# Optimization experiments

Measured on AMD Instinct MI355X. Metric: run time of the kernel, lower is better.

## Reference

```python
import jax, jax.numpy as jnp
import numpy as np

MODE1 = 12
MODE2 = 12
WIDTH = 64
L = 10
DEPTH = 4
PAD = 9
EPS = 1e-5


def conv1x1(x, w, b):
    # x: (B,Ci,H,W), w: (Co,Ci), b: (Co,)
    return jnp.einsum('oi,bihw->bohw', w, x) + b[None, :, None, None]


def group_norm(x, gamma, beta, groups=2):
    B, C, H, W = x.shape
    xg = x.reshape(B, groups, C // groups, H, W)
    mu = xg.mean(axis=(2, 3, 4), keepdims=True)
    var = xg.var(axis=(2, 3, 4), keepdims=True)
    xn = ((xg - mu) * jax.lax.rsqrt(var + EPS)).reshape(B, C, H, W)
    return xn * gamma[None, :, None, None] + beta[None, :, None, None]


def spectral_conv(x, w1, w2):
    # x: (B,Ci,H,W); w1,w2: (Ci,Co,m1,m2,2) real/imag stacked
    B, Ci, H, W = x.shape
    Co = w1.shape[1]
    x_ft = jnp.fft.rfft2(x)  # (B,Ci,H,W//2+1) complex
    w1c = w1[..., 0] + 1j * w1[..., 1]
    w2c = w2[..., 0] + 1j * w2[..., 1]
    t1 = jnp.einsum('bixy,ioxy->boxy', x_ft[:, :, :MODE1, :MODE2], w1c)
    t2 = jnp.einsum('bixy,ioxy->boxy', x_ft[:, :, -MODE1:, :MODE2], w2c)
    out_ft = jnp.zeros((B, Co, H, W // 2 + 1), dtype=x_ft.dtype)
    out_ft = out_ft.at[:, :, :MODE1, :MODE2].set(t1)
    out_ft = out_ft.at[:, :, -MODE1:, :MODE2].set(t2)
    return jnp.fft.irfft2(out_ft, s=(H, W))


def mlp_block(x, w1, b1, g, bt, w2, b2):
    x = conv1x1(x, w1, b1)
    x = group_norm(x, g, bt)
    x = jax.nn.gelu(x, approximate=False)
    return conv1x1(x, w2, b2)


def get_grid(B, S):
    gx = jnp.linspace(0.0, 1.0, S, dtype=jnp.float32)
    gy = jnp.linspace(0.0, 1.0, S, dtype=jnp.float32)
    gridx = jnp.broadcast_to(gx[None, :, None, None], (B, S, S, 1))
    gridy = jnp.broadcast_to(gy[None, None, :, None], (B, S, S, 1))
    return jnp.concatenate([gridx, gridy], axis=-1)  # (B,S,S,2)


def pos_encoding(grid):
    # grid: (B,S,S,2) -> (B,S,S,4L); cos over all L then sin over all L,
    # within each L the 2 grid channels stay adjacent (matches torch cat order)
    freqs = (jnp.pi * (2.0 ** jnp.arange(L))).astype(jnp.float32)  # (L,)
    phase = grid[..., None, :] * freqs[:, None]  # (B,S,S,L,2)
    B, S1, S2 = grid.shape[:3]
    phase = phase.reshape(B, S1, S2, L * 2)
    return jnp.concatenate([jnp.cos(phase), jnp.sin(phase)], axis=-1)


def setup_inputs() -> dict:
    key = jax.random.key(0)
    ks = jax.random.split(key, 24)
    B, S = 8, 192
    Cin = 3 + 4 * L  # 43
    Wd = WIDTH
    scale = 1.0 / (Wd * Wd)
    d = {}
    d['x'] = jax.random.normal(ks[0], (B, S, S, 1), dtype=jnp.float32)
    d['Wp'] = jax.random.normal(ks[1], (Cin, Wd), dtype=jnp.float32) / np.sqrt(Cin)
    d['bp'] = jnp.zeros((Wd,), dtype=jnp.float32)
    d['sw1'] = scale * jax.random.uniform(ks[2], (DEPTH, Wd, Wd, MODE1, MODE2, 2), dtype=jnp.float32)
    d['sw2'] = scale * jax.random.uniform(ks[3], (DEPTH, Wd, Wd, MODE1, MODE2, 2), dtype=jnp.float32)
    d['m1w'] = jax.random.normal(ks[4], (DEPTH, Wd, Wd), dtype=jnp.float32) / np.sqrt(Wd)
    d['m1b'] = jnp.zeros((DEPTH, Wd), dtype=jnp.float32)
    d['mg'] = jnp.ones((DEPTH, Wd), dtype=jnp.float32)
    d['mbt'] = jnp.zeros((DEPTH, Wd), dtype=jnp.float32)
    d['m2w'] = jax.random.normal(ks[5], (DEPTH, Wd, Wd), dtype=jnp.float32) / np.sqrt(Wd)
    d['m2b'] = jnp.zeros((DEPTH, Wd), dtype=jnp.float32)
    d['ww'] = jax.random.normal(ks[6], (DEPTH, Wd, Wd), dtype=jnp.float32) / np.sqrt(Wd)
    d['wb'] = jnp.zeros((DEPTH, Wd), dtype=jnp.float32)
    d['ng'] = jnp.ones((DEPTH, Wd), dtype=jnp.float32)
    d['nb'] = jnp.zeros((DEPTH, Wd), dtype=jnp.float32)
    Wq = Wd * 4
    d['q1w'] = jax.random.normal(ks[7], (Wq, Wd), dtype=jnp.float32) / np.sqrt(Wd)
    d['q1b'] = jnp.zeros((Wq,), dtype=jnp.float32)
    d['qg'] = jnp.ones((Wq,), dtype=jnp.float32)
    d['qbt'] = jnp.zeros((Wq,), dtype=jnp.float32)
    d['q2w'] = jax.random.normal(ks[8], (1, Wq), dtype=jnp.float32) / np.sqrt(Wq)
    d['q2b'] = jnp.zeros((1,), dtype=jnp.float32)
    return d


def reference(x, Wp, bp, sw1, sw2, m1w, m1b, mg, mbt, m2w, m2b, ww, wb, ng, nb,
              q1w, q1b, qg, qbt, q2w, q2b):
    B, S = x.shape[0], x.shape[1]
    grid = get_grid(B, S)
    pe = pos_encoding(grid)
    h = jnp.concatenate([x, grid, pe], axis=-1)  # (B,S,S,43)
    h = h @ Wp + bp  # lift
    h = h.transpose(0, 3, 1, 2)  # (B,W,S,S)
    h = jnp.pad(h, ((0, 0), (0, 0), (0, PAD), (0, PAD)))
    for i in range(DEPTH):
        x1 = spectral_conv(h, sw1[i], sw2[i])
        x1 = mlp_block(x1, m1w[i], m1b[i], mg[i], mbt[i], m2w[i], m2b[i])
        x2 = conv1x1(h, ww[i], wb[i])
        x2 = group_norm(x2, ng[i], nb[i])
        h = x1 + x2
        if i != DEPTH - 1:
            h = jax.nn.gelu(h, approximate=False)
    h = h[..., :-PAD, :-PAD]
    h = mlp_block(h, q1w, q1b, qg, qbt, q2w, q2b)
    return h.transpose(0, 2, 3, 1)  # (B,S,S,1)
```

## Files before the change

### kernel.cpp

```cpp
#include <hip/hip_runtime.h>
#include <hip/hip_bf16.h>
#include <math.h>


#define NN 201
#define SS 192
#define NPIX 40401
#define QPIX 36864
#define BB 8
#define GNB 80
#define XWPL 1234944
#define PI_F 3.14159265358979323846f

typedef __hip_bfloat16 bf16;
typedef __attribute__((ext_vector_type(8))) short s8v;
typedef __attribute__((ext_vector_type(4))) float f32x4;

__device__ __forceinline__ float gelu_f(float x){
  float x2 = x*x;
  float t  = fmaf(x2, 0.0713548162f, 1.5957691216f);
  float e  = __expf(-x*t);
  return x*__builtin_amdgcn_rcpf(1.0f+e);
}
__device__ __forceinline__ float b2f(bf16 v){ return __bfloat162float(v); }
// ... 178 lines not shown
    v.w = (unsigned)f2bu(v6) | ((unsigned)f2bu(v7)<<16);
    dst[i]=v;
  }
}

__global__ void __launch_bounds__(256) k_dftw(const bf16* __restrict__ A,
        const unsigned short* __restrict__ T2PK, bf16* __restrict__ XWb){
  int tid=threadIdx.x, wid=tid>>6, l=tid&63;
  int m_=l&15, g=l>>4;
  int R = blockIdx.x*4 + wid;
  const bf16* row = A + (size_t)R*NN*64;
  f32x4 acc[2][4];
  #pragma unroll
  for(int mt=0;mt<2;mt++){
    #pragma unroll
    for(int nt=0;nt<4;nt++) acc[mt][nt]=f32x4{0.f,0.f,0.f,0.f};
  }
  for(int chunk=0;chunk<7;chunk++){
    int wbase = chunk*32 + g*8;
    s8v bf[4];
    if(chunk<6){
      #pragma unroll
      for(int nt=0;nt<4;nt++){
        s8v f;
        #pragma unroll
        for(int j=0;j<8;j++){
          unsigned short v;
          bf16 hv = row[(size_t)(wbase+j)*64 + 16*nt + m_];
          __builtin_memcpy(&v,&hv,2);
          f[j]=(short)v;
        }
        bf[nt]=f;
      }
    } else {
      #pragma unroll
      for(int nt=0;nt<4;nt++){
        s8v f;
        #pragma unroll
        for(int j=0;j<8;j++){
          unsigned short v=0;
          if(wbase+j<NN){
            bf16 hv = row[(size_t)(wbase+j)*64 + 16*nt + m_];
            __builtin_memcpy(&v,&hv,2);
          }
          f[j]=(short)v;
        }
        bf[nt]=f;
      }
    }
    #pragma unroll
    for(int mt=0;mt<2;mt++){
      s8v af = *(const s8v*)(T2PK + (size_t)(mt*7+chunk)*512 + l*8);
      #pragma unroll
      for(int nt=0;nt<4;nt++)
        acc[mt][nt]=__builtin_amdgcn_mfma_f32_16x16x32_bf16(af,bf[nt],acc[mt][nt],0,0,0);
    }
  }
  int bb = R/NN, h = R - bb*NN;
  #pragma unroll
  for(int mt=0;mt<2;mt++){
    #pragma unroll
    for(int nt=0;nt<4;nt++){
      #pragma unroll
      for(int e=0;e<4;e++){
        int kx24 = mt*16 + 4*g + e;
        if(kx24<24){
          int plane = kx24&1, kx = kx24>>1;
          XWb[(size_t)plane*XWPL + (((size_t)bb*12+kx)*201 + h)*64 + 16*nt + m_]
            = f2b(acc[mt][nt][e]);
        }
      }
    }
  }
}

__global__ void __launch_bounds__(256) k_dfthM(const bf16* __restrict__ XWb,
        const unsigned short* __restrict__ T3PK, float* __restrict__ XF){
  int kx=blockIdx.x, b=blockIdx.y, zh=blockIdx.z;
  int tid=threadIdx.x, wid=tid>>6, l=tid&63;
  int m_=l&15, g=l>>4;
  if(wid>=3) return;
  const bf16* base = XWb + (((size_t)b*12+kx)*201)*64;
  f32x4 acc0=f32x4{0.f,0.f,0.f,0.f}, acc1=f32x4{0.f,0.f,0.f,0.f};
  for(int chunk=0;chunk<13;chunk++){
    s8v bf0, bf1;
    #pragma unroll
    for(int nt2=0;nt2<2;nt2++){
      int c = 16*(zh*2+nt2) + m_;
      s8v f;
      #pragma unroll
      for(int j=0;j<8;j++){
        int k = chunk*32 + g*8 + j;
        unsigned short v=0;
        if(k<402){
          int h = (k<201)? k : (k-201);
          size_t poff = (k<201)? 0 : (size_t)XWPL;
          bf16 hv = base[poff + (size_t)h*64 + c];
          __builtin_memcpy(&v,&hv,2);
        }
        f[j]=(short)v;
      }
      if(nt2==0) bf0=f; else bf1=f;
    }
    s8v af = *(const s8v*)(T3PK + (size_t)(wid*13+chunk)*512 + l*8);
    acc0=__builtin_amdgcn_mfma_f32_16x16x32_bf16(af,bf0,acc0,0,0,0);
    acc1=__builtin_amdgcn_mfma_f32_16x16x32_bf16(af,bf1,acc1,0,0,0);
  }
  #pragma unroll
  for(int nt2=0;nt2<2;nt2++){
    f32x4 a = (nt2==0)? acc0 : acc1;
    int c = 16*(zh*2+nt2) + m_;
    #pragma unroll
    for(int e2=0;e2<4;e2++){
      int m = wid*16 + 4*g + e2;
      int j24 = m>>1, comp = m&1;
      XF[(size_t)(j24*12+kx)*1024 + ((size_t)b*64+c)*2 + comp] = a[e2];
    }
  }
}

__global__ void __launch_bounds__(512) k_modemix(const float* __restrict__ XF,
     const unsigned short* __restrict__ WT, float* __restrict__ XO){
  __shared__ float sx[1024];
  __shared__ float swr[4096], swi[4096];
  int m=blockIdx.x;
  int tid=threadIdx.x;
  sx[tid]     = XF[(size_t)m*1024+tid];
  sx[tid+512] = XF[(size_t)m*1024+tid+512];
  const unsigned short* wr = WT + (size_t)m*8192;
  const unsigned short* wi = wr + 4096;
  for(int io=tid;io<4096;io+=512){
    swr[io]=bu2f(wr[io]);
    swi[io]=bu2f(wi[io]);
  }
  __syncthreads();
  int b=tid>>6, o=tid&63;
  const float* xb = sx + b*128;
  float re0=0.f,re1=0.f,im0=0.f,im1=0.f;
  #pragma unroll 8
  for(int i=0;i<64;i+=2){
    float a=xb[2*i], b2=xb[2*i+1];
    float c=swr[i*64+o], d=swi[i*64+o];
    re0 = fmaf(a,c, fmaf(-b2,d, re0));
    im0 = fmaf(a,d, fmaf( b2,c, im0));
    float a1=xb[2*i+2], b3=xb[2*i+3];
    float c1=swr[(i+1)*64+o], d1=swi[(i+1)*64+o];
    re1 = fmaf(a1,c1, fmaf(-b3,d1, re1));
    im1 = fmaf(a1,d1, fmaf( b3,c1, im1));
  }
  XO[2*((size_t)m*512+tid)]  =re0+re1;
  XO[2*((size_t)m*512+tid)+1]=im0+im1;
}

__global__ void __launch_bounds__(256) k_ispec(const float* __restrict__ XO,
        const float* __restrict__ tab, const unsigned short* __restrict__ TPK,
        bf16* __restrict__ C){
  __shared__ float2 yl[12][64];
  __shared__ float2 cs13[13];
  int R=blockIdx.x;
  int b=R/NN, h=R-b*NN;
  int tid=threadIdx.x;
  if(tid<13) cs13[tid]=((const float2*)tab)[tid*NN+h];
  __syncthreads();
  const float sc = 1.0f/40401.0f;
  #pragma unroll
  for(int it=0;it<3;it++){
    int item = tid + 256*it;
    int kx = item>>6, o = item&63;
    float re0=0.f,im0=0.f,re1=0.f,im1=0.f;
    #pragma unroll
    for(int j=0;j<24;j+=2){
      {
        int k2=(j<12)?j:24-j;
        float sgn=(j<12)?1.0f:-1.0f;
        float2 xo = *(const float2*)(XO + 2*(((size_t)(j*12+kx)*512) + b*64 + o));
        float2 cs = cs13[k2];
        float cc=cs.x, s2=sgn*cs.y;
        re0 = fmaf(xo.x,cc, fmaf(-xo.y,s2, re0));
        im0 = fmaf(xo.x,s2, fmaf( xo.y,cc, im0));
      }
      {
        int j1=j+1;
        int k2=(j1<12)?j1:24-j1;
        float sgn=(j1<12)?1.0f:-1.0f;
        float2 xo = *(const float2*)(XO + 2*(((size_t)(j1*12+kx)*512) + b*64 + o));
        float2 cs = cs13[k2];
        float cc=cs.x, s2=sgn*cs.y;
        re1 = fmaf(xo.x,cc, fmaf(-xo.y,s2, re1));
        im1 = fmaf(xo.x,s2, fmaf( xo.y,cc, im1));
      }
    }
    float fr = (kx==0)? sc : 2.0f*sc;
    float fi = (kx==0)? sc : -2.0f*sc;
    yl[kx][o] = float2{ (re0+re1)*fr, (im0+im1)*fi };
  }
  __syncthreads();
  int wid=tid>>6, l=tid&63, m_=l&15, g=l>>4;
  int o = wid*16 + m_;
  s8v bfr;
  #pragma unroll
  for(int j=0;j<4;j++){
    float2 v = yl[4*g+j][o];
    bfr[2*j]   = (short)f2bu(v.x);
    bfr[2*j+1] = (short)f2bu(v.y);
  }
  bf16* cp = C + (size_t)R*NN*64;
  #pragma unroll
  for(int wt=0; wt<13; wt++){
    s8v af = *(const s8v*)(TPK + (size_t)wt*512 + l*8);
    f32x4 acc = f32x4{0.f,0.f,0.f,0.f};
    acc = __builtin_amdgcn_mfma_f32_16x16x32_bf16(af, bfr, acc, 0,0,0);
    #pragma unroll
    for(int e=0;e<4;e++){
      int w = wt*16 + 4*g + e;
      if(w<NN) cp[(size_t)w*64 + o] = f2b(acc[e]);
    }
  }
}

__global__ void __launch_bounds__(256) k_gramC(const float* __restrict__ XO,
        float* __restrict__ GCp, float* __restrict__ SC){
  __shared__ unsigned short V[64][72];
  int chunk=blockIdx.x, b=blockIdx.y, tid=threadIdx.x;
  const float s1=1.0f/201.0f;
  const float r2=0.70710678118f;
  const float q2=1.41421356237f;
  #pragma unroll
  for(int it=0;it<16;it++){
    int e = tid + it*256;
    int fl=e>>6, ch=e&63;
    int f = chunk*64 + fl;
    int base = b*64+ch;
    float v=0.f;
    if(f<528){
      int comp=f&1, kxm=f>>1;
      int kx0=kxm/24;
      int kx=1+kx0, m=kxm-kx0*24;
      v = q2*XO[2*((size_t)(m*12+kx)*512 + base)+comp];
    } else if(f==528){
      v = XO[2*(size_t)base];
    } else if(f<551){
      int q=f-529; int mm=1+(q>>1);
      const float* p1 = XO + 2*((size_t)(mm*12)*512 + base);
      const float* p2 = XO + 2*((size_t)((24-mm)*12)*512 + base);
      v = ((q&1)==0)? r2*(p1[0]+p2[0]) : r2*(p1[1]-p2[1]);
    } else if(f==551){
      v = r2*XO[2*((size_t)(144)*512 + base)];
    } else if(f==552){
      v = r2*XO[2*((size_t)(144)*512 + base)+1];
    }
    V[ch][fl]=f2bu(v*s1);
  }
  __syncthreads();
  int wid=tid>>6, l=tid&63, m_=l&15, g=l>>4;
  f32x4 acc[4];
  #pragma unroll
  for(int mt=0;mt<4;mt++) acc[mt]=f32x4{0.f,0.f,0.f,0.f};
  #pragma unroll
  for(int kc=0;kc<2;kc++){
    s8v bfr = *(const s8v*)&V[16*wid+m_][kc*32+8*g];
    #pragma unroll
    for(int mt=0;mt<4;mt++){
      s8v afr = *(const s8v*)&V[16*mt+m_][kc*32+8*g];
      acc[mt]=__builtin_amdgcn_mfma_f32_16x16x32_bf16(afr,bfr,acc[mt],0,0,0);
    }
  }
  float* gb = GCp + ((size_t)(b*9+chunk))*4096;
  #pragma unroll
  for(int mt=0;mt<4;mt++){
    #pragma unroll
    for(int e=0;e<4;e++)
      gb[(size_t)(16*mt+4*g+e)*64 + 16*wid + m_] = acc[mt][e];
  }
  if(chunk==0 && tid<64) SC[b*64+tid] = XO[2*(size_t)(b*64+tid)];
}

__global__ void __launch_bounds__(256) k_gramp(const bf16* __restrict__ X,
        float* __restrict__ Gpart, float* __restrict__ Spart, int HR, int WR){
  int b = blockIdx.y, blk = blockIdx.x;
  int npix = HR*WR;
  int tid=threadIdx.x, wid=tid>>6, l=tid&63;
  int m_=l&15, g=l>>4;
  int slab = blk*4 + wid;
  const bf16* xb = X + (size_t)b*NPIX*64;
  f32x4 acc[4][4];
  #pragma unroll
  for(int mt=0;mt<4;mt++){
    #pragma unroll
    for(int nt=0;nt<4;nt++) acc[mt][nt]=f32x4{0.f,0.f,0.f,0.f};
  }
  float cs[4]={0.f,0.f,0.f,0.f};
  for(int kc=0;kc<16;kc++){
    int pbase = slab*512 + kc*32 + g*8;
    int hh0=0, ww0=0;
    if(WR!=NN){ hh0 = pbase/WR; ww0 = pbase - hh0*WR; }
    const bf16* ptr[8];
    #pragma unroll
    for(int jj=0;jj<8;jj++){
      int p = pbase + jj;
      int gp;
      if(WR==NN) gp = p;
      else {
        int ww2 = ww0 + jj;
        int hh  = hh0;
        if(ww2>=WR){ ww2-=WR; hh++; }
        gp = hh*NN + ww2;
      }
      ptr[jj] = (p<npix) ? (xb + (size_t)gp*64) : (const bf16*)0;
    }
    s8v fr[4];
    #pragma unroll
    for(int t=0;t<4;t++){
      s8v f;
      float s=0.f;
      #pragma unroll
      for(int jj=0;jj<8;jj++){
        unsigned short v=0;
        if(ptr[jj]){ bf16 hv = ptr[jj][16*t+m_]; __builtin_memcpy(&v,&hv,2); }
        f[jj]=(short)v;
        s += bu2f(v);
      }
      fr[t]=f;
      cs[t]+=s;
    }
    #pragma unroll
    for(int nt=0;nt<4;nt++){
      #pragma unroll
      for(int mt=0;mt<4;mt++)
        acc[mt][nt]=__builtin_amdgcn_mfma_f32_16x16x32_bf16(fr[mt],fr[nt],acc[mt][nt],0,0,0);
    }
  }
  float* gp_ = Gpart + ((size_t)(b*GNB + slab))*4096;
  #pragma unroll
  for(int mt=0;mt<4;mt++){
    #pragma unroll
    for(int nt=0;nt<4;nt++){
      #pragma unroll
      for(int e=0;e<4;e++)
        gp_[(size_t)(16*mt + 4*g + e)*64 + 16*nt + m_] = acc[mt][nt][e];
    }
  }
  #pragma unroll
  for(int t=0;t<4;t++){
    float s=cs[t];
    s += __shfl_xor(s,16,64);
    s += __shfl_xor(s,32,64);
    if(g==0) Spart[((size_t)(b*GNB+slab))*64 + 16*t + m_] = s;
  }
}

__global__ void __launch_bounds__(256) k_gramr(const float* __restrict__ Gpart,
        const float* __restrict__ Spart, float* __restrict__ Gfin,
        float* __restrict__ Sfin, int nblk){
  int b = blockIdx.y;
  int idx = blockIdx.x*256 + threadIdx.x;
  float s0=0.f,s1=0.f,s2=0.f,s3=0.f;
  int k=0;
  for(;k+3<nblk;k+=4){
    s0 += Gpart[((size_t)b*GNB + k  )*4096 + idx];
    s1 += Gpart[((size_t)b*GNB + k+1)*4096 + idx];
    s2 += Gpart[((size_t)b*GNB + k+2)*4096 + idx];
    s3 += Gpart[((size_t)b*GNB + k+3)*4096 + idx];
  }
  for(;k<nblk;k++) s0 += Gpart[((size_t)b*GNB + k)*4096 + idx];
  Gfin[(size_t)b*4096 + idx] = (s0+s1)+(s2+s3);
  if(blockIdx.x==0 && threadIdx.x<64){
    float ss=0.f;
    for(int j=0;j<nblk;j++) ss += Spart[((size_t)b*GNB + j)*64 + threadIdx.x];
    Sfin[b*64 + threadIdx.x]=ss;
  }
}

__global__ void __launch_bounds__(256) k_statsA(
        const float* __restrict__ GCp, const float* __restrict__ SC,
        const float* __restrict__ Gfin, const float* __restrict__ Sfin,
        const float* __restrict__ m1wl, const float* __restrict__ m1bl,
        const float* __restrict__ wwl,  const float* __restrict__ wbl,
        float* __restrict__ TSTAT, float* __restrict__ USTAT){
  __shared__ float Gs[4096];
  __shared__ float Ss[64];
  __shared__ float rs[256], rq[256];
  int zb2=blockIdx.x;
  int zb=zb2>>1, grp=zb2&1;
  int t=threadIdx.x;
  if(zb<8){
    #pragma unroll
    for(int e=0;e<16;e++){
      float s=0.f;
      #pragma unroll
      for(int q=0;q<9;q++) s += GCp[((size_t)(zb*9+q))*4096 + t*16+e];
      Gs[t*16+e]=s;
    }
    if(t<64) Ss[t]=SC[zb*64+t];
  } else {
    const float* GS = Gfin + (size_t)(zb-8)*4096;
    #pragma unroll
    for(int e=0;e<16;e++) Gs[t*16+e]=GS[t*16+e];
    if(t<64) Ss[t]=Sfin[(zb-8)*64+t];
  }
  __syncthreads();
  const float* W    = (zb<8)? m1wl : wwl;
  const float* bias = (zb<8)? m1bl : wbl;
  float* stat       = (zb<8)? TSTAT : USTAT;
  int b = (zb<8)? zb : zb-8;
  int o = grp*32 + (t&31);
  int sl = t>>5;
  float w[64];
  #pragma unroll
  for(int j2=0;j2<64;j2++) w[j2]=bu2f(f2bu(W[(size_t)o*64+j2]));
  const float* Gr = Gs + (size_t)(sl*8)*64;
  float quad=0.f;
  #pragma unroll
  for(int r=0;r<8;r++){
    const float* gr = Gr + r*64;
    float tt=0.f;
    #pragma unroll
    for(int j2=0;j2<64;j2++) tt += gr[j2]*w[j2];
    quad += w[sl*8+r]*tt;
  }
  float sm=0.f, sq=quad;
  if(sl==0){
    float dot=0.f;
    #pragma unroll
    for(int j2=0;j2<64;j2++) dot += w[j2]*Ss[j2];
    float bo = bias[o];
    float Nf = (float)NPIX;
    sm = dot + Nf*bo;
    sq += 2.f*bo*dot + Nf*bo*bo;
  }
  rs[t]=sm; rq[t]=sq;
  __syncthreads();
  if(t<32){
    float s2=0.f,q2=0.f;
    #pragma unroll
    for(int k=0;k<8;k++){ s2+=rs[t+32*k]; q2+=rq[t+32*k]; }
    for(int off=16;off>0;off>>=1){
      s2 += __shfl_down(s2,off,32);
      q2 += __shfl_down(q2,off,32);
    }
    if(t==0){
      float invN = 1.f/((float)NPIX*32.f);
      float mean = s2*invN;
      float var = q2*invN - mean*mean;
      stat[b*4+grp*2]   = mean;
      stat[b*4+grp*2+1] = rsqrtf(fmaxf(var,0.f)+1e-5f);
    }
  }
}

__global__ void __launch_bounds__(256) k_statsQ(const float* __restrict__ Gfin,
        const float* __restrict__ Sfin,
        const float* __restrict__ W, const float* __restrict__ bias,
        float* __restrict__ QP){
  __shared__ float Gs[4096];
  __shared__ float Ss[64];
  __shared__ float rs[256], rq[256];
  int b=blockIdx.x, z=blockIdx.y, t=threadIdx.x;
  #pragma unroll
  for(int e=0;e<16;e++) Gs[t*16+e]=Gfin[(size_t)b*4096 + t*16+e];
  if(t<64) Ss[t]=Sfin[b*64+t];
  __syncthreads();
  int o = z*64 + (t&63);
  int sl = t>>6;
  float w[64];
  #pragma unroll
  for(int j2=0;j2<64;j2++) w[j2]=bu2f(f2bu(W[(size_t)o*64+j2]));
  const float* Gr = Gs + (size_t)(sl*16)*64;
  float quad=0.f;
  #pragma unroll
  for(int r=0;r<16;r++){
    const float* gr = Gr + r*64;
    float tt=0.f;
    #pragma unroll
    for(int j2=0;j2<64;j2++) tt += gr[j2]*w[j2];
    quad += w[sl*16+r]*tt;
  }
  float sm=0.f, sq=quad;
  if(sl==0){
    float dot=0.f;
    #pragma unroll
    for(int j2=0;j2<64;j2++) dot += w[j2]*Ss[j2];
    float bo=bias[o];
    float Nf=(float)QPIX;
    sm = dot + Nf*bo;
    sq += 2.f*bo*dot + Nf*bo*bo;
  }
  rs[t]=sm; rq[t]=sq;
  __syncthreads();
  if(t<64){
    float s2 = rs[t]+rs[t+64]+rs[t+128]+rs[t+192];
    float q2 = rq[t]+rq[t+64]+rq[t+128]+rq[t+192];
    for(int off=32;off>0;off>>=1){
      s2 += __shfl_down(s2,off,64);
      q2 += __shfl_down(q2,off,64);
    }
    if(t==0){
      int g = z>>1;
      atomicAdd(&QP[b*4+g*2],   s2);
      atomicAdd(&QP[b*4+g*2+1], q2);
    }
  }
}

__global__ void k_qfin(const float* __restrict__ QP, float* __restrict__ QSTAT){
  int t=threadIdx.x;
  if(t>=16) return;
  int b=t>>1, g=t&1;
  float s=QP[b*4+g*2], ss=QP[b*4+g*2+1];
  float invN=1.f/((float)QPIX*128.f);
  float mean=s*invN, var=ss*invN-mean*mean;
  QSTAT[b*4+g*2]   = mean;
  QSTAT[b*4+g*2+1] = rsqrtf(fmaxf(var,0.f)+1e-5f);
}

__global__ void __launch_bounds__(128) k_fuse(const bf16* __restrict__ Cb,
    bf16* __restrict__ A,
    const unsigned short* __restrict__ wp1, const float* __restrict__ m1b,
    const float* __restrict__ mg,  const float* __restrict__ mbt,
    const unsigned short* __restrict__ wp2, const float* __restrict__ m2b,
    const unsigned short* __restrict__ wpw, const float* __restrict__ wbk,
    const float* __restrict__ ng,  const float* __restrict__ nb,
    const float* __restrict__ tstat, const float* __restrict__ ustat, int last){
  __shared__ unsigned short vlds[2][64][72];
  int tid=threadIdx.x;
  int wid=tid>>6, l=tid&63;
  int m_=l&15, g=l>>4;
  int b=blockIdx.y;
  int p0=blockIdx.x*128 + wid*64;
  const bf16* cbb = Cb + (size_t)b*NPIX*64;
  const bf16* ab  = A  + (size_t)b*NPIX*64;

  s8v af[4][2];
  f32x4 acc[4][4];

  #pragma unroll
  for(int mt=0;mt<4;mt++){
    #pragma unroll
    for(int kh=0;kh<2;kh++)
      af[mt][kh]=*(const s8v*)(wp1 + (mt*2+kh)*512 + l*8);
    float4 b4 = *(const float4*)(m1b + 16*mt + 4*g);
    #pragma unroll
    for(int nt=0;nt<4;nt++) acc[mt][nt]=f32x4{b4.x,b4.y,b4.z,b4.w};
  }
  #pragma unroll
  for(int nt=0;nt<4;nt++){
    int p = p0 + 16*nt + m_;
    int pc = p<NPIX? p : NPIX-1;
    const s8v* xb = (const s8v*)(cbb + (size_t)pc*64);
    s8v b0 = xb[g], b1 = xb[4+g];
    #pragma unroll
    for(int mt=0;mt<4;mt++){
      acc[mt][nt]=__builtin_amdgcn_mfma_f32_16x16x32_bf16(af[mt][0],b0,acc[mt][nt],0,0,0);
      acc[mt][nt]=__builtin_amdgcn_mfma_f32_16x16x32_bf16(af[mt][1],b1,acc[mt][nt],0,0,0);
    }
  }
  {
    float tm0=tstat[b*4],tr0=tstat[b*4+1],tm1=tstat[b*4+2],tr1=tstat[b*4+3];
    #pragma unroll
    for(int mt=0;mt<4;mt++){
      float4 g4 = *(const float4*)(mg  + 16*mt + 4*g);
      float4 t4 = *(const float4*)(mbt + 16*mt + 4*g);
      float mn = (mt<2)? tm0 : tm1;
      float rs = (mt<2)? tr0 : tr1;
      float ax=rs*g4.x, ay=rs*g4.y, az=rs*g4.z, aw=rs*g4.w;
      float cx=t4.x-mn*ax, cy=t4.y-mn*ay, cz=t4.z-mn*az, cw=t4.w-mn*aw;
      #pragma unroll
      for(int nt=0;nt<4;nt++){
        int pl = 16*nt + m_;
        f32x4 t = acc[mt][nt];
        float v0 = gelu_f(fmaf(t[0],ax,cx));
        float v1 = gelu_f(fmaf(t[1],ay,cy));
        float v2 = gelu_f(fmaf(t[2],az,cz));
        float v3 = gelu_f(fmaf(t[3],aw,cw));
        uint2 pk;
        pk.x = (unsigned)f2bu(v0) | ((unsigned)f2bu(v1)<<16);
        pk.y = (unsigned)f2bu(v2) | ((unsigned)f2bu(v3)<<16);
        *(uint2*)&vlds[wid][pl][16*mt+4*g] = pk;
      }
    }
  }
  #pragma unroll
  for(int mt=0;mt<4;mt++){
    #pragma unroll
    for(int kh=0;kh<2;kh++)
      af[mt][kh]=*(const s8v*)(wpw + (mt*2+kh)*512 + l*8);
    float4 b4 = *(const float4*)(wbk + 16*mt + 4*g);
    #pragma unroll
    for(int nt=0;nt<4;nt++) acc[mt][nt]=f32x4{b4.x,b4.y,b4.z,b4.w};
  }
  #pragma unroll
  for(int nt=0;nt<4;nt++){
    int p = p0 + 16*nt + m_;
    int pc = p<NPIX? p : NPIX-1;
    const s8v* xb = (const s8v*)(ab + (size_t)pc*64);
    s8v b0 = xb[g], b1 = xb[4+g];
    #pragma unroll
    for(int mt=0;mt<4;mt++){
      acc[mt][nt]=__builtin_amdgcn_mfma_f32_16x16x32_bf16(af[mt][0],b0,acc[mt][nt],0,0,0);
      acc[mt][nt]=__builtin_amdgcn_mfma_f32_16x16x32_bf16(af[mt][1],b1,acc[mt][nt],0,0,0);
    }
  }
  {
    float um0=ustat[b*4],ur0=ustat[b*4+1],um1=ustat[b*4+2],ur1=ustat[b*4+3];
    #pragma unroll
    for(int mt=0;mt<4;mt++){
      float4 n4 = *(const float4*)(ng  + 16*mt + 4*g);
      float4 nb4= *(const float4*)(nb  + 16*mt + 4*g);
      float4 m24= *(const float4*)(m2b + 16*mt + 4*g);
      float mn = (mt<2)? um0 : um1;
      float rs = (mt<2)? ur0 : ur1;
      float ax=rs*n4.x, ay=rs*n4.y, az=rs*n4.z, aw=rs*n4.w;
      float cx=m24.x+nb4.x-mn*ax, cy=m24.y+nb4.y-mn*ay;
      float cz=m24.z+nb4.z-mn*az, cw=m24.w+nb4.w-mn*aw;
      #pragma unroll
      for(int nt=0;nt<4;nt++){
        f32x4 u = acc[mt][nt];
        u[0] = fmaf(u[0],ax,cx);
        u[1] = fmaf(u[1],ay,cy);
        u[2] = fmaf(u[2],az,cz);
        u[3] = fmaf(u[3],aw,cw);
        acc[mt][nt]=u;
      }
    }
  }
  #pragma unroll
  for(int mt=0;mt<4;mt++){
    #pragma unroll
    for(int kh=0;kh<2;kh++)
      af[mt][kh]=*(const s8v*)(wp2 + (mt*2+kh)*512 + l*8);
  }
  #pragma unroll
  for(int nt=0;nt<4;nt++){
    int pl = 16*nt + m_;
    const s8v* vp = (const s8v*)&vlds[wid][pl][0];
    s8v b0 = vp[g], b1 = vp[4+g];
    #pragma unroll
    for(int mt=0;mt<4;mt++){
      acc[mt][nt]=__builtin_amdgcn_mfma_f32_16x16x32_bf16(af[mt][0],b0,acc[mt][nt],0,0,0);
      acc[mt][nt]=__builtin_amdgcn_mfma_f32_16x16x32_bf16(af[mt][1],b1,acc[mt][nt],0,0,0);
    }
  }
  #pragma unroll
  for(int nt=0;nt<4;nt++){
    int p = p0 + 16*nt + m_;
    if(p>=NPIX) continue;
    bf16* dp = A + ((size_t)b*NPIX + p)*64;
    #pragma unroll
    for(int mt=0;mt<4;mt++){
      f32x4 h = acc[mt][nt];
      float h0=h[0],h1=h[1],h2=h[2],h3=h[3];
      if(!last){ h0=gelu_f(h0); h1=gelu_f(h1); h2=gelu_f(h2); h3=gelu_f(h3); }
      uint2 pk;
      pk.x = (unsigned)f2bu(h0) | ((unsigned)f2bu(h1)<<16);
      pk.y = (unsigned)f2bu(h2) | ((unsigned)f2bu(h3)<<16);
      *(uint2*)(dp + 16*mt + 4*g) = pk;
    }
  }
}

__global__ void __launch_bounds__(256) k_qout(const bf16* __restrict__ A,
    const unsigned short* __restrict__ qpack, const float* __restrict__ q1b,
    const float* __restrict__ qg, const float* __restrict__ qbt,
    const float* __restrict__ q2w, const float* __restrict__ q2b,
    const float* __restrict__ qstat, float* __restrict__ out){
  __shared__ unsigned short xq[128][72];
  __shared__ float part[4][128];
  int tid=threadIdx.x;
  int wid=tid>>6, l=tid&63;
  int m_=l&15, g=l>>4;
  int b=blockIdx.y;
  int px0=blockIdx.x*128;
  {
    int p = px0 + (tid>>1);
    int half = tid&1;
    int hh=p/SS, ww2=p-hh*SS;
    const uint4* src=(const uint4*)(A + (((size_t)b*NPIX) + (size_t)hh*NN + ww2)*64 + half*32);
    uint4* drow=(uint4*)&xq[tid>>1][half*32];
    #pragma unroll
    for(int i=0;i<4;i++) drow[i]=src[i];
  }
  __syncthreads();
  int oc=wid;
  const unsigned short* wp = qpack + (size_t)oc*4096;
  s8v af[4][2];
  f32x4 bi4[4];
  float4 a4[4], c4[4], w4[4];
  float m0=qstat[b*4],r0=qstat[b*4+1],m1=qstat[b*4+2],r1=qstat[b*4+3];
  float mn=(oc<2)?m0:m1, rs=(oc<2)?r0:r1;
  #pragma unroll
  for(int mt=0;mt<4;mt++){
    #pragma unroll
    for(int kh=0;kh<2;kh++)
      af[mt][kh]=*(const s8v*)(wp + (mt*2+kh)*512 + l*8);
    float4 b4=*(const float4*)(q1b + 64*oc + 16*mt + 4*g);
    bi4[mt]=f32x4{b4.x,b4.y,b4.z,b4.w};
    float4 g4=*(const float4*)(qg  + 64*oc + 16*mt + 4*g);
    float4 t4=*(const float4*)(qbt + 64*oc + 16*mt + 4*g);
    w4[mt]=*(const float4*)(q2w + 64*oc + 16*mt + 4*g);
    a4[mt]=float4{rs*g4.x, rs*g4.y, rs*g4.z, rs*g4.w};
    c4[mt]=float4{t4.x-mn*a4[mt].x, t4.y-mn*a4[mt].y, t4.z-mn*a4[mt].z, t4.w-mn*a4[mt].w};
  }
  #pragma unroll
  for(int nt=0;nt<8;nt++){
    const s8v* vp = (const s8v*)&xq[16*nt+m_][0];
    s8v b0=vp[g], b1=vp[4+g];
    f32x4 acc[4];
    #pragma unroll
    for(int mt=0;mt<4;mt++) acc[mt]=bi4[mt];
    #pragma unroll
    for(int mt=0;mt<4;mt++){
      acc[mt]=__builtin_amdgcn_mfma_f32_16x16x32_bf16(af[mt][0],b0,acc[mt],0,0,0);
      acc[mt]=__builtin_amdgcn_mfma_f32_16x16x32_bf16(af[mt][1],b1,acc[mt],0,0,0);
    }
    float pp=0.f;
    #pragma unroll
    for(int mt=0;mt<4;mt++){
      f32x4 t=acc[mt];
      pp += gelu_f(fmaf(t[0],a4[mt].x,c4[mt].x))*w4[mt].x;
      pp += gelu_f(fmaf(t[1],a4[mt].y,c4[mt].y))*w4[mt].y;
      pp += gelu_f(fmaf(t[2],a4[mt].z,c4[mt].z))*w4[mt].z;
      pp += gelu_f(fmaf(t[3],a4[mt].w,c4[mt].w))*w4[mt].w;
    }
    pp += __shfl_xor(pp,16,64);
    pp += __shfl_xor(pp,32,64);
    if(g==0) part[wid][16*nt+m_]=pp;
  }
  __syncthreads();
  if(tid<128)
    out[(size_t)b*QPIX + px0 + tid] =
        q2b[0] + part[0][tid]+part[1][tid]+part[2][tid]+part[3][tid];
}

extern "C" void kernel_launch(void* const* d_in, const int* in_sizes, int n_in,
                              void* d_out, int out_size, void* d_ws, size_t ws_size,
                              hipStream_t stream){
  const float* x   = (const float*)d_in[0];
  const float* Wp  = (const float*)d_in[1];
  const float* bp  = (const float*)d_in[2];
  const float* sw1 = (const float*)d_in[3];
  const float* sw2 = (const float*)d_in[4];
  const float* m1w = (const float*)d_in[5];
  const float* m1b = (const float*)d_in[6];
  const float* mg  = (const float*)d_in[7];
  const float* mbt = (const float*)d_in[8];
  const float* m2w = (const float*)d_in[9];
  const float* m2b = (const float*)d_in[10];
  const float* ww  = (const float*)d_in[11];
  const float* wb  = (const float*)d_in[12];
  const float* ng  = (const float*)d_in[13];
  const float* nb  = (const float*)d_in[14];
  const float* q1w = (const float*)d_in[15];
  const float* q1b = (const float*)d_in[16];
  const float* qg  = (const float*)d_in[17];
  const float* qbt = (const float*)d_in[18];
  const float* q2w = (const float*)d_in[19];
  const float* q2b = (const float*)d_in[20];
  float* out = (float*)d_out;

  char* w8 = (char*)d_ws;
  const size_t ACT_B = (size_t)64*BB*NPIX*sizeof(bf16);
  bf16*  A    = (bf16*)(w8);
  bf16*  Cb   = (bf16*)(w8 + ACT_B);
  float* SPEC = (float*)(w8 + 2*ACT_B);
  float* XF   = (float*)(w8 + 2*ACT_B + 9879552);
  float* XO   = (float*)(w8 + 2*ACT_B + 9879552 + 1179648);
  float* TB   = (float*)(w8 + 2*ACT_B + 9879552 + 2*1179648);
  char*  g8   = w8 + 2*ACT_B + 9879552 + 2*1179648 + 20992;
  float* TSTAT= (float*)g8;
  float* USTAT= TSTAT + 32;
  float* QSTAT= USTAT + 32;
  float* UxT  = QSTAT + 32;
  float* UyT  = UxT + 12288;
  unsigned short* WPK = (unsigned short*)(UyT + 12288);
  float* GFIN = (float*)(WPK + 16*4096);
  float* SFIN = GFIN + 8*4096;
  float* SC   = SFIN + 8*64;
  unsigned short* TPK = (unsigned short*)(SC + 8*64);
  unsigned short* T2PK = TPK + 6656;
  unsigned short* T3PK = T2PK + 7168;
  float* QP   = (float*)(T3PK + 19968);
  float* GCp  = QP + 32;
  unsigned short* WT = (unsigned short*)(GCp + (size_t)8*9*4096);
  bf16*  XWb  = (bf16*)SPEC;
  float* Gpart = SPEC;
  float* Spart = Gpart + (size_t)8*GNB*4096;
  size_t needed = (size_t)(2*ACT_B) + 9879552 + 2*1179648 + 20992
                + 3*32*4 + 2*12288*4 + 16*4096*2 + (8*4096+2*8*64)*4
                + 13312 + 14336 + 39936 + 128
                + (size_t)8*9*4096*4 + (size_t)288*8192*2;
  if(ws_size < needed) return;

  k_tab<<<11,256,0,stream>>>(TB);
  k_tpack<<<26,256,0,stream>>>(TB, TPK);
  k_tpack2<<<28,256,0,stream>>>(TB, T2PK);
  k_tpack3<<<78,256,0,stream>>>(TB, T3PK);
  k_pretab<<<dim3(192,2),64,0,stream>>>(Wp, bp, UxT, UyT);
  k_wpack<<<16,256,0,stream>>>(m1w, m2w, ww, q1w, WPK);
  k_encoder<<<dim3(158,BB),256,0,stream>>>(x, Wp, UxT, UyT, A);

  for(int l=0;l<4;l++){
    const float* sw1l = sw1 + (size_t)l*1179648;
    const float* sw2l = sw2 + (size_t)l*1179648;
    k_dftw<<<402,256,0,stream>>>(A, T2PK, XWb);
    k_dfthM<<<dim3(12,BB,2),256,0,stream>>>(XWb, T3PK, XF);
    k_wtrans<<<dim3(64,5,2),256,0,stream>>>(sw1l, sw2l, WT);
    k_modemix<<<288,512,0,stream>>>(XF, WT, XO);
    k_ispec<<<1608,256,0,stream>>>(XO, TB, TPK, Cb);
    k_gramC<<<dim3(9,BB),256,0,stream>>>(XO, GCp, SC);
    k_gramp<<<dim3(20,BB),256,0,stream>>>(A, Gpart, Spart, NN, NN);
    k_gramr<<<dim3(16,BB),256,0,stream>>>(Gpart, Spart, GFIN, SFIN, 80);
    k_statsA<<<32,256,0,stream>>>(GCp, SC, GFIN, SFIN,
          m1w + (size_t)l*4096, m1b + l*64, ww + (size_t)l*4096, wb + l*64,
          TSTAT, USTAT);
    k_fuse<<<dim3(316,BB),128,0,stream>>>(Cb, A,
          WPK + (size_t)(l*3+0)*4096, m1b + l*64, mg + l*64, mbt + l*64,
          WPK + (size_t)(l*3+1)*4096, m2b + l*64,
          WPK + (size_t)(l*3+2)*4096, wb  + l*64, ng + l*64, nb + l*64,
          TSTAT, USTAT, (l==3)?1:0);
  }

  k_gramp<<<dim3(18,BB),256,0,stream>>>(A, Gpart, Spart, SS, SS);
  k_gramr<<<dim3(16,BB),256,0,stream>>>(Gpart, Spart, GFIN, SFIN, 72);
  hipMemsetAsync(QP, 0, 32*sizeof(float), stream);
  k_statsQ<<<dim3(BB,4),256,0,stream>>>(GFIN, SFIN, q1w, q1b, QP);
  k_qfin<<<1,16,0,stream>>>(QP, QSTAT);
  k_qout<<<dim3(288,BB),256,0,stream>>>(A, WPK + (size_t)12*4096, q1b,
          qg, qbt, q2w, q2b, QSTAT, out);
}
```

Baseline: 820.5 us.

## Fuse inverse spectral transform into per-row MLP/skip fusion kernel via LDS

Merges the inverse-DFT kernel into the channel-MLP/skip fusion kernel. Each block now builds its spectral output row (201 pixels x 64 channels) directly in shared memory and consumes it there, so the bf16 intermediate Cb no longer makes a round trip through global memory, and one launch per layer goes away. The cost is a large LDS buffer per block, and row-aligned tiling where one wave handles four 16-pixel tiles and the others three, which leaves some padding waste. It also splits the qout reduction into a tree sum to shorten the dependency chain.

```diff
diff --git a/kernel.cpp b/kernel.cpp
--- a/kernel.cpp
+++ b/kernel.cpp
@@ -354,15 +354,23 @@
   XO[2*((size_t)m*512+tid)+1]=im0+im1;
 }
 
-__global__ void __launch_bounds__(256) k_ispec(const float* __restrict__ XO,
-        const float* __restrict__ tab, const unsigned short* __restrict__ TPK,
-        bf16* __restrict__ C){
+__global__ void __launch_bounds__(256) k_ifuse(const float* __restrict__ XO,
+    const float* __restrict__ tab, const unsigned short* __restrict__ TPK,
+    bf16* __restrict__ A,
+    const unsigned short* __restrict__ wp1, const float* __restrict__ m1b,
+    const float* __restrict__ mg,  const float* __restrict__ mbt,
+    const unsigned short* __restrict__ wp2, const float* __restrict__ m2b,
+    const unsigned short* __restrict__ wpw, const float* __restrict__ wbk,
+    const float* __restrict__ ng,  const float* __restrict__ nb,
+    const float* __restrict__ tstat, const float* __restrict__ ustat, int last){
+  __shared__ unsigned short cb[208][72];
   __shared__ float2 yl[12][64];
   __shared__ float2 cs13[13];
   int R=blockIdx.x;
   int b=R/NN, h=R-b*NN;
   int tid=threadIdx.x;
   if(tid<13) cs13[tid]=((const float2*)tab)[tid*NN+h];
+  for(int i=tid;i<252;i+=256) ((unsigned*)cb)[7236+i]=0u;
   __syncthreads();
   const float sc = 1.0f/40401.0f;
   #pragma unroll
@@ -398,24 +406,157 @@
   }
   __syncthreads();
   int wid=tid>>6, l=tid&63, m_=l&15, g=l>>4;
-  int o = wid*16 + m_;
-  s8v bfr;
-  #pragma unroll
-  for(int j=0;j<4;j++){
-    float2 v = yl[4*g+j][o];
-    bfr[2*j]   = (short)f2bu(v.x);
-    bfr[2*j+1] = (short)f2bu(v.y);
-  }
-  bf16* cp = C + (size_t)R*NN*64;
-  #pragma unroll
-  for(int wt=0; wt<13; wt++){
-    s8v af = *(const s8v*)(TPK + (size_t)wt*512 + l*8);
-    f32x4 acc = f32x4{0.f,0.f,0.f,0.f};
-    acc = __builtin_amdgcn_mfma_f32_16x16x32_bf16(af, bfr, acc, 0,0,0);
-    #pragma unroll
-    for(int e=0;e<4;e++){
-      int w = wt*16 + 4*g + e;
-      if(w<NN) cp[(size_t)w*64 + o] = f2b(acc[e]);
+  {
+    int o = wid*16 + m_;
+    s8v bfr;
+    #pragma unroll
+    for(int j=0;j<4;j++){
+      float2 v = yl[4*g+j][o];
+      bfr[2*j]   = (short)f2bu(v.x);
+      bfr[2*j+1] = (short)f2bu(v.y);
+    }
+    #pragma unroll
+    for(int wt=0; wt<13; wt++){
+      s8v af0 = *(const s8v*)(TPK + (size_t)wt*512 + l*8);
+      f32x4 acc0 = f32x4{0.f,0.f,0.f,0.f};
+      acc0 = __builtin_amdgcn_mfma_f32_16x16x32_bf16(af0, bfr, acc0, 0,0,0);
+      #pragma unroll
+      for(int e=0;e<4;e++){
+        int w = wt*16 + 4*g + e;
+        if(w<NN) cb[w][o] = f2bu(acc0[e]);
+      }
+    }
+  }
+  __syncthreads();
+  const bf16* ab = A + (size_t)b*NPIX*64;
+  int ntv = (wid==0)? 4 : 3;
+  s8v af[4][2];
+  f32x4 acc[4][4];
+  #pragma unroll
+  for(int mt=0;mt<4;mt++){
+    #pragma unroll
+    for(int kh=0;kh<2;kh++)
+      af[mt][kh]=*(const s8v*)(wp1 + (mt*2+kh)*512 + l*8);
+    float4 b4 = *(const float4*)(m1b + 16*mt + 4*g);
+    #pragma unroll
+    for(int nt=0;nt<4;nt++) acc[mt][nt]=f32x4{b4.x,b4.y,b4.z,b4.w};
+  }
+  #pragma unroll
+  for(int nt=0;nt<4;nt++){
+    if(nt>=ntv) continue;
+    int row = 16*(wid+4*nt) + m_;
+    const s8v* vp = (const s8v*)&cb[row][0];
+    s8v b0 = vp[g], b1 = vp[4+g];
+    #pragma unroll
+    for(int mt=0;mt<4;mt++){
+      acc[mt][nt]=__builtin_amdgcn_mfma_f32_16x16x32_bf16(af[mt][0],b0,acc[mt][nt],0,0,0);
+      acc[mt][nt]=__builtin_amdgcn_mfma_f32_16x16x32_bf16(af[mt][1],b1,acc[mt][nt],0,0,0);
+    }
+  }
+  {
+    float tm0=tstat[b*4],tr0=tstat[b*4+1],tm1=tstat[b*4+2],tr1=tstat[b*4+3];
+    #pragma unroll
+    for(int mt=0;mt<4;mt++){
+      float4 g4 = *(const float4*)(mg  + 16*mt + 4*g);
+      float4 t4 = *(const float4*)(mbt + 16*mt + 4*g);
+      float mn = (mt<2)? tm0 : tm1;
+      float rs = (mt<2)? tr0 : tr1;
+      float ax=rs*g4.x, ay=rs*g4.y, az=rs*g4.z, aw=rs*g4.w;
+      float cx=t4.x-mn*ax, cy=t4.y-mn*ay, cz=t4.z-mn*az, cw=t4.w-mn*aw;
+      #pragma unroll
+      for(int nt=0;nt<4;nt++){
+        if(nt>=ntv) continue;
+        int row = 16*(wid+4*nt) + m_;
+        f32x4 t = acc[mt][nt];
+        float v0 = gelu_f(fmaf(t[0],ax,cx));
+        float v1 = gelu_f(fmaf(t[1],ay,cy));
+        float v2 = gelu_f(fmaf(t[2],az,cz));
+        float v3 = gelu_f(fmaf(t[3],aw,cw));
+        uint2 pk;
+        pk.x = (unsigned)f2bu(v0) | ((unsigned)f2bu(v1)<<16);
+        pk.y = (unsigned)f2bu(v2) | ((unsigned)f2bu(v3)<<16);
+        *(uint2*)&cb[row][16*mt+4*g] = pk;
+      }
+    }
+  }
+  #pragma unroll
+  for(int mt=0;mt<4;mt++){
+    #pragma unroll
+    for(int kh=0;kh<2;kh++)
+      af[mt][kh]=*(const s8v*)(wpw + (mt*2+kh)*512 + l*8);
+    float4 b4 = *(const float4*)(wbk + 16*mt + 4*g);
+    #pragma unroll
+    for(int nt=0;nt<4;nt++) acc[mt][nt]=f32x4{b4.x,b4.y,b4.z,b4.w};
+  }
+  #pragma unroll
+  for(int nt=0;nt<4;nt++){
+    if(nt>=ntv) continue;
+    int w = 16*(wid+4*nt) + m_;
+    int wc = (w<NN)? w : (NN-1);
+    const s8v* xb = (const s8v*)(ab + (size_t)(h*NN + wc)*64);
+    s8v b0 = xb[g], b1 = xb[4+g];
+    #pragma unroll
+    for(int mt=0;mt<4;mt++){
+      acc[mt][nt]=__builtin_amdgcn_mfma_f32_16x16x32_bf16(af[mt][0],b0,acc[mt][nt],0,0,0);
+      acc[mt][nt]=__builtin_amdgcn_mfma_f32_16x16x32_bf16(af[mt][1],b1,acc[mt][nt],0,0,0);
+    }
+  }
+  {
+    float um0=ustat[b*4],ur0=ustat[b*4+1],um1=ustat[b*4+2],ur1=ustat[b*4+3];
+    #pragma unroll
+    for(int mt=0;mt<4;mt++){
+      float4 n4 = *(const float4*)(ng  + 16*mt + 4*g);
+      float4 nb4= *(const float4*)(nb  + 16*mt + 4*g);
+      float4 m24= *(const float4*)(m2b + 16*mt + 4*g);
+      float mn = (mt<2)? um0 : um1;
+      float rs = (mt<2)? ur0 : ur1;
+      float ax=rs*n4.x, ay=rs*n4.y, az=rs*n4.z, aw=rs*n4.w;
+      float cx=m24.x+nb4.x-mn*ax, cy=m24.y+nb4.y-mn*ay;
+      float cz=m24.z+nb4.z-mn*az, cw=m24.w+nb4.w-mn*aw;
+      #pragma unroll
+      for(int nt=0;nt<4;nt++){
+        f32x4 u = acc[mt][nt];
+        u[0] = fmaf(u[0],ax,cx);
+        u[1] = fmaf(u[1],ay,cy);
+        u[2] = fmaf(u[2],az,cz);
+        u[3] = fmaf(u[3],aw,cw);
+        acc[mt][nt]=u;
+      }
+    }
+  }
+  #pragma unroll
+  for(int mt=0;mt<4;mt++){
+    #pragma unroll
+    for(int kh=0;kh<2;kh++)
+      af[mt][kh]=*(const s8v*)(wp2 + (mt*2+kh)*512 + l*8);
+  }
+  #pragma unroll
+  for(int nt=0;nt<4;nt++){
+    if(nt>=ntv) continue;
+    int row = 16*(wid+4*nt) + m_;
+    const s8v* vp = (const s8v*)&cb[row][0];
+    s8v b0 = vp[g], b1 = vp[4+g];
+    #pragma unroll
+    for(int mt=0;mt<4;mt++){
+      acc[mt][nt]=__builtin_amdgcn_mfma_f32_16x16x32_bf16(af[mt][0],b0,acc[mt][nt],0,0,0);
+      acc[mt][nt]=__builtin_amdgcn_mfma_f32_16x16x32_bf16(af[mt][1],b1,acc[mt][nt],0,0,0);
+    }
+  }
+  #pragma unroll
+  for(int nt=0;nt<4;nt++){
+    if(nt>=ntv) continue;
+    int w = 16*(wid+4*nt) + m_;
+    if(w>=NN) continue;
+    bf16* dp = A + ((size_t)b*NPIX + (size_t)h*NN + w)*64;
+    #pragma unroll
+    for(int mt=0;mt<4;mt++){
+      f32x4 hh = acc[mt][nt];
+      float h0=hh[0],h1=hh[1],h2=hh[2],h3=hh[3];
+      if(!last){ h0=gelu_f(h0); h1=gelu_f(h1); h2=gelu_f(h2); h3=gelu_f(h3); }
+      uint2 pk;
+      pk.x = (unsigned)f2bu(h0) | ((unsigned)f2bu(h1)<<16);
+      pk.y = (unsigned)f2bu(h2) | ((unsigned)f2bu(h3)<<16);
+      *(uint2*)(dp + 16*mt + 4*g) = pk;
     }
   }
 }
@@ -715,151 +856,6 @@
   QSTAT[b*4+g*2+1] = rsqrtf(fmaxf(var,0.f)+1e-5f);
 }
 
-__global__ void __launch_bounds__(128) k_fuse(const bf16* __restrict__ Cb,
-    bf16* __restrict__ A,
-    const unsigned short* __restrict__ wp1, const float* __restrict__ m1b,
-    const float* __restrict__ mg,  const float* __restrict__ mbt,
-    const unsigned short* __restrict__ wp2, const float* __restrict__ m2b,
-    const unsigned short* __restrict__ wpw, const float* __restrict__ wbk,
-    const float* __restrict__ ng,  const float* __restrict__ nb,
-    const float* __restrict__ tstat, const float* __restrict__ ustat, int last){
-  __shared__ unsigned short vlds[2][64][72];
-  int tid=threadIdx.x;
-  int wid=tid>>6, l=tid&63;
-  int m_=l&15, g=l>>4;
-  int b=blockIdx.y;
-  int p0=blockIdx.x*128 + wid*64;
-  const bf16* cbb = Cb + (size_t)b*NPIX*64;
-  const bf16* ab  = A  + (size_t)b*NPIX*64;
-
-  s8v af[4][2];
-  f32x4 acc[4][4];
-
-  #pragma unroll
-  for(int mt=0;mt<4;mt++){
-    #pragma unroll
-    for(int kh=0;kh<2;kh++)
-      af[mt][kh]=*(const s8v*)(wp1 + (mt*2+kh)*512 + l*8);
-    float4 b4 = *(const float4*)(m1b + 16*mt + 4*g);
-    #pragma unroll
-    for(int nt=0;nt<4;nt++) acc[mt][nt]=f32x4{b4.x,b4.y,b4.z,b4.w};
-  }
-  #pragma unroll
-  for(int nt=0;nt<4;nt++){
-    int p = p0 + 16*nt + m_;
-    int pc = p<NPIX? p : NPIX-1;
-    const s8v* xb = (const s8v*)(cbb + (size_t)pc*64);
-    s8v b0 = xb[g], b1 = xb[4+g];
-    #pragma unroll
-    for(int mt=0;mt<4;mt++){
-      acc[mt][nt]=__builtin_amdgcn_mfma_f32_16x16x32_bf16(af[mt][0],b0,acc[mt][nt],0,0,0);
-      acc[mt][nt]=__builtin_amdgcn_mfma_f32_16x16x32_bf16(af[mt][1],b1,acc[mt][nt],0,0,0);
-    }
-  }
-  {
-    float tm0=tstat[b*4],tr0=tstat[b*4+1],tm1=tstat[b*4+2],tr1=tstat[b*4+3];
-    #pragma unroll
-    for(int mt=0;mt<4;mt++){
-      float4 g4 = *(const float4*)(mg  + 16*mt + 4*g);
-      float4 t4 = *(const float4*)(mbt + 16*mt + 4*g);
-      float mn = (mt<2)? tm0 : tm1;
-      float rs = (mt<2)? tr0 : tr1;
-      float ax=rs*g4.x, ay=rs*g4.y, az=rs*g4.z, aw=rs*g4.w;
-      float cx=t4.x-mn*ax, cy=t4.y-mn*ay, cz=t4.z-mn*az, cw=t4.w-mn*aw;
-      #pragma unroll
-      for(int nt=0;nt<4;nt++){
-        int pl = 16*nt + m_;
-        f32x4 t = acc[mt][nt];
-        float v0 = gelu_f(fmaf(t[0],ax,cx));
-        float v1 = gelu_f(fmaf(t[1],ay,cy));
-        float v2 = gelu_f(fmaf(t[2],az,cz));
-        float v3 = gelu_f(fmaf(t[3],aw,cw));
-        uint2 pk;
-        pk.x = (unsigned)f2bu(v0) | ((unsigned)f2bu(v1)<<16);
-        pk.y = (unsigned)f2bu(v2) | ((unsigned)f2bu(v3)<<16);
-        *(uint2*)&vlds[wid][pl][16*mt+4*g] = pk;
-      }
-    }
-  }
-  #pragma unroll
-  for(int mt=0;mt<4;mt++){
-    #pragma unroll
-    for(int kh=0;kh<2;kh++)
-      af[mt][kh]=*(const s8v*)(wpw + (mt*2+kh)*512 + l*8);
-    float4 b4 = *(const float4*)(wbk + 16*mt + 4*g);
-    #pragma unroll
-    for(int nt=0;nt<4;nt++) acc[mt][nt]=f32x4{b4.x,b4.y,b4.z,b4.w};
-  }
-  #pragma unroll
-  for(int nt=0;nt<4;nt++){
-    int p = p0 + 16*nt + m_;
-    int pc = p<NPIX? p : NPIX-1;
-    const s8v* xb = (const s8v*)(ab + (size_t)pc*64);
-    s8v b0 = xb[g], b1 = xb[4+g];
-    #pragma unroll
-    for(int mt=0;mt<4;mt++){
-      acc[mt][nt]=__builtin_amdgcn_mfma_f32_16x16x32_bf16(af[mt][0],b0,acc[mt][nt],0,0,0);
-      acc[mt][nt]=__builtin_amdgcn_mfma_f32_16x16x32_bf16(af[mt][1],b1,acc[mt][nt],0,0,0);
-    }
-  }
-  {
-    float um0=ustat[b*4],ur0=ustat[b*4+1],um1=ustat[b*4+2],ur1=ustat[b*4+3];
-    #pragma unroll
-    for(int mt=0;mt<4;mt++){
-      float4 n4 = *(const float4*)(ng  + 16*mt + 4*g);
-      float4 nb4= *(const float4*)(nb  + 16*mt + 4*g);
-      float4 m24= *(const float4*)(m2b + 16*mt + 4*g);
-      float mn = (mt<2)? um0 : um1;
-      float rs = (mt<2)? ur0 : ur1;
-      float ax=rs*n4.x, ay=rs*n4.y, az=rs*n4.z, aw=rs*n4.w;
-      float cx=m24.x+nb4.x-mn*ax, cy=m24.y+nb4.y-mn*ay;
-      float cz=m24.z+nb4.z-mn*az, cw=m24.w+nb4.w-mn*aw;
-      #pragma unroll
-      for(int nt=0;nt<4;nt++){
-        f32x4 u = acc[mt][nt];
-        u[0] = fmaf(u[0],ax,cx);
-        u[1] = fmaf(u[1],ay,cy);
-        u[2] = fmaf(u[2],az,cz);
-        u[3] = fmaf(u[3],aw,cw);
-        acc[mt][nt]=u;
-      }
-    }
-  }
-  #pragma unroll
-  for(int mt=0;mt<4;mt++){
-    #pragma unroll
-    for(int kh=0;kh<2;kh++)
-      af[mt][kh]=*(const s8v*)(wp2 + (mt*2+kh)*512 + l*8);
-  }
-  #pragma unroll
-  for(int nt=0;nt<4;nt++){
-    int pl = 16*nt + m_;
-    const s8v* vp = (const s8v*)&vlds[wid][pl][0];
-    s8v b0 = vp[g], b1 = vp[4+g];
-    #pragma unroll
-    for(int mt=0;mt<4;mt++){
-      acc[mt][nt]=__builtin_amdgcn_mfma_f32_16x16x32_bf16(af[mt][0],b0,acc[mt][nt],0,0,0);
-      acc[mt][nt]=__builtin_amdgcn_mfma_f32_16x16x32_bf16(af[mt][1],b1,acc[mt][nt],0,0,0);
-    }
-  }
-  #pragma unroll
-  for(int nt=0;nt<4;nt++){
-    int p = p0 + 16*nt + m_;
-    if(p>=NPIX) continue;
-    bf16* dp = A + ((size_t)b*NPIX + p)*64;
-    #pragma unroll
-    for(int mt=0;mt<4;mt++){
-      f32x4 h = acc[mt][nt];
-      float h0=h[0],h1=h[1],h2=h[2],h3=h[3];
-      if(!last){ h0=gelu_f(h0); h1=gelu_f(h1); h2=gelu_f(h2); h3=gelu_f(h3); }
-      uint2 pk;
-      pk.x = (unsigned)f2bu(h0) | ((unsigned)f2bu(h1)<<16);
-      pk.y = (unsigned)f2bu(h2) | ((unsigned)f2bu(h3)<<16);
-      *(uint2*)(dp + 16*mt + 4*g) = pk;
-    }
-  }
-}
-
 __global__ void __launch_bounds__(256) k_qout(const bf16* __restrict__ A,
     const unsigned short* __restrict__ qpack, const float* __restrict__ q1b,
     const float* __restrict__ qg, const float* __restrict__ qbt,
@@ -914,15 +910,17 @@
       acc[mt]=__builtin_amdgcn_mfma_f32_16x16x32_bf16(af[mt][0],b0,acc[mt],0,0,0);
       acc[mt]=__builtin_amdgcn_mfma_f32_16x16x32_bf16(af[mt][1],b1,acc[mt],0,0,0);
     }
-    float pp=0.f;
+    float ppv[4];
     #pragma unroll
     for(int mt=0;mt<4;mt++){
       f32x4 t=acc[mt];
-      pp += gelu_f(fmaf(t[0],a4[mt].x,c4[mt].x))*w4[mt].x;
-      pp += gelu_f(fmaf(t[1],a4[mt].y,c4[mt].y))*w4[mt].y;
-      pp += gelu_f(fmaf(t[2],a4[mt].z,c4[mt].z))*w4[mt].z;
-      pp += gelu_f(fmaf(t[3],a4[mt].w,c4[mt].w))*w4[mt].w;
-    }
+      float q0 = gelu_f(fmaf(t[0],a4[mt].x,c4[mt].x))*w4[mt].x;
+      float q1 = gelu_f(fmaf(t[1],a4[mt].y,c4[mt].y))*w4[mt].y;
+      float q2 = gelu_f(fmaf(t[2],a4[mt].z,c4[mt].z))*w4[mt].z;
+      float q3 = gelu_f(fmaf(t[3],a4[mt].w,c4[mt].w))*w4[mt].w;
+      ppv[mt] = (q0+q1)+(q2+q3);
+    }
+    float pp = (ppv[0]+ppv[1])+(ppv[2]+ppv[3]);
     pp += __shfl_xor(pp,16,64);
     pp += __shfl_xor(pp,32,64);
     if(g==0) part[wid][16*nt+m_]=pp;
@@ -991,6 +989,7 @@
                 + 13312 + 14336 + 39936 + 128
                 + (size_t)8*9*4096*4 + (size_t)288*8192*2;
   if(ws_size < needed) return;
+  (void)Cb;
 
   k_tab<<<11,256,0,stream>>>(TB);
   k_tpack<<<26,256,0,stream>>>(TB, TPK);
@@ -1007,14 +1006,13 @@
     k_dfthM<<<dim3(12,BB,2),256,0,stream>>>(XWb, T3PK, XF);
     k_wtrans<<<dim3(64,5,2),256,0,stream>>>(sw1l, sw2l, WT);
     k_modemix<<<288,512,0,stream>>>(XF, WT, XO);
-    k_ispec<<<1608,256,0,stream>>>(XO, TB, TPK, Cb);
     k_gramC<<<dim3(9,BB),256,0,stream>>>(XO, GCp, SC);
     k_gramp<<<dim3(20,BB),256,0,stream>>>(A, Gpart, Spart, NN, NN);
     k_gramr<<<dim3(16,BB),256,0,stream>>>(Gpart, Spart, GFIN, SFIN, 80);
     k_statsA<<<32,256,0,stream>>>(GCp, SC, GFIN, SFIN,
           m1w + (size_t)l*4096, m1b + l*64, ww + (size_t)l*4096, wb + l*64,
           TSTAT, USTAT);
-    k_fuse<<<dim3(316,BB),128,0,stream>>>(Cb, A,
+    k_ifuse<<<1608,256,0,stream>>>(XO, TB, TPK, A,
           WPK + (size_t)(l*3+0)*4096, m1b + l*64, mg + l*64, mbt + l*64,
           WPK + (size_t)(l*3+1)*4096, m2b + l*64,
           WPK + (size_t)(l*3+2)*4096, wb  + l*64, ng + l*64, nb + l*64,
```

Result: no change. 817.7 us (-0.3%).
